# Optimization experiments

Measured on AMD Instinct MI355X. Metric: run time of the kernel, lower is better.

Reference implementation:

```python
import jax, jax.numpy as jnp
import numpy as np

D_IN = 1024
N_HEADS = 16
DEPTH = D_IN // N_HEADS
SCALE = float(np.sqrt(DEPTH))


def setup_inputs() -> dict:
    key = jax.random.key(0)
    ks = jax.random.split(key, 11)
    B, S = 4, 1024
    s = 0.02
    return {
        "q": jax.random.normal(ks[0], (B, S, D_IN), jnp.float32),
        "k": jax.random.normal(ks[1], (B, S, D_IN), jnp.float32),
        "v": jax.random.normal(ks[2], (B, S, D_IN), jnp.float32),
        "mask": jnp.zeros((1, 1, S, S), jnp.float32),
        "wq_w": jax.random.normal(ks[3], (D_IN, D_IN), jnp.float32) * s,
        "wq_b": jax.random.normal(ks[4], (D_IN,), jnp.float32) * s,
        "wk_w": jax.random.normal(ks[5], (D_IN, D_IN), jnp.float32) * s,
        "wk_b": jax.random.normal(ks[6], (D_IN,), jnp.float32) * s,
        "wv_w": jax.random.normal(ks[7], (D_IN, D_IN), jnp.float32) * s,
        "wv_b": jax.random.normal(ks[8], (D_IN,), jnp.float32) * s,
        "pl_w": jax.random.normal(ks[9], (D_IN, D_IN), jnp.float32) * s,
        "pl_b": jax.random.normal(ks[10], (D_IN,), jnp.float32) * s,
    }


def _split_heads(x):
    # [B, S, D] -> [B, H, S, depth]
    B, S, _ = x.shape
    return x.reshape(B, S, N_HEADS, DEPTH).transpose(0, 2, 1, 3)


def reference(q, k, v, mask, wq_w, wq_b, wk_w, wk_b, wv_w, wv_b, pl_w, pl_b):
    # torch Linear: y = x @ W.T + b
    qh = _split_heads(q @ wq_w.T + wq_b)
    kh = _split_heads(k @ wk_w.T + wk_b)
    vh = _split_heads(v @ wv_w.T + wv_b)
    # [B, H, Sq, Sk]
    logits = jnp.einsum("bhqd,bhkd->bhqk", qh, kh) / SCALE
    logits = logits + mask * (-1e9)
    weights = jax.nn.softmax(logits, axis=-1)
    attn = jnp.einsum("bhqk,bhkd->bhqd", weights, vh)
    B = q.shape[0]
    attn = attn.transpose(0, 2, 1, 3).reshape(B, -1, D_IN)
    return attn @ pl_w.T + pl_b
```

## Files before the change

kernel.cpp:

```cpp
#include <hip/hip_runtime.h>
#include <stdint.h>

#define B_ 4
#define S_ 1024
#define DMODEL 1024
#define H_ 16
#define DP_ 64

typedef __attribute__((ext_vector_type(8))) short short8;
typedef __attribute__((ext_vector_type(4))) float floatx4;
typedef __attribute__((ext_vector_type(16))) float floatx16;
typedef __attribute__((ext_vector_type(8))) unsigned short ushort8;
typedef __attribute__((ext_vector_type(4))) unsigned short ushort4v;
typedef __attribute__((ext_vector_type(4))) unsigned int uintx4;

#define LOG2E 1.44269504088896f

__device__ __forceinline__ unsigned short f2bf(float x) {
    union { float f; unsigned int u; } c; c.f = x;
    unsigned int r = c.u + 0x7FFFu + ((c.u >> 16) & 1u);
    return (unsigned short)(r >> 16);
}
__device__ __forceinline__ float bf2f(unsigned short b) {
    union { float f; unsigned int u; } c; c.u = ((unsigned int)b) << 16;
    return c.f;
}
__device__ __forceinline__ unsigned pack2(float lo, float hi) {
    union { float f; unsigned int u; } a, b; a.f = lo; b.f = hi;
    return ((b.u + 0x8000u) & 0xFFFF0000u) | ((a.u + 0x8000u) >> 16);
}

#if __has_builtin(__builtin_amdgcn_exp2f)
#define EXP2(x) __builtin_amdgcn_exp2f(x)
#else
#define EXP2(x) exp2f(x)
#endif

#define GLDS16(gp, lp) __builtin_amdgcn_global_load_lds( \
    (const __attribute__((address_space(1))) void*)(gp),  \
    (__attribute__((address_space(3))) void*)(lp), 16, 0, 0)

__global__ __launch_bounds__(256) void convert_all(
    const float* __restrict__ q, const float* __restrict__ k, const float* __restrict__ v,
    const float* __restrict__ wq, const float* __restrict__ wk, const float* __restrict__ wv,
    const float* __restrict__ wp, const float* __restrict__ mask,
    unsigned short* __restrict__ ws)
{
    const unsigned g = blockIdx.x * 256u + threadIdx.x;
    const float* s; unsigned short* d; unsigned off; float sc = 1.0f;
    if (g < 524288u)        { s = q;  d = ws;            off = g; }
    else if (g < 1048576u)  { s = k;  d = ws + 4194304;  off = g - 524288u; }
    else if (g < 1572864u)  { s = v;  d = ws + 8388608;  off = g - 1048576u; }
    else if (g < 1703936u)  { s = wq; d = ws + 12582912; off = g - 1572864u; }
    else if (g < 1835008u)  { s = wk; d = ws + 13631488; off = g - 1703936u; }
    else if (g < 1966080u)  { s = wv; d = ws + 14680064; off = g - 1835008u; }
    else if (g < 2097152u)  { s = wp; d = ws + 15728640; off = g - 1966080u; }
    else { s = mask; d = ws + 16777216; off = g - 2097152u; sc = -1e9f * LOG2E; }
    const floatx4 a = ((const floatx4*)s)[(size_t)off * 2];
    const floatx4 b = ((const floatx4*)s)[(size_t)off * 2 + 1];
    ushort8 r;
    r[0] = f2bf(a[0] * sc); r[1] = f2bf(a[1] * sc); r[2] = f2bf(a[2] * sc); r[3] = f2bf(a[3] * sc);
    r[4] = f2bf(b[0] * sc); r[5] = f2bf(b[1] * sc); r[6] = f2bf(b[2] * sc); r[7] = f2bf(b[3] * sc);
    ((ushort8*)d)[off] = r;
}

template<bool SWAP>
__device__ __forceinline__ void gemm_body(
    const unsigned short* __restrict__ X, const unsigned short* __restrict__ W,
    const int row0, const int col0,
    unsigned short* Xs, unsigned short* Ws, floatx4* acc)
{
    const int tid = threadIdx.x, w = tid >> 6, lane = tid & 63;
    const int l15 = lane & 15, l4 = lane >> 4;
    const int wr = w >> 1, wc = w & 1;
    const int srow = lane >> 3;
    const int sgrp = (lane & 7) ^ srow;
    auto* XsL = (__attribute__((address_space(3))) unsigned short*)Xs;
    auto* WsL = (__attribute__((address_space(3))) unsigned short*)Ws;

    for (int it = 0; it < 16; it++) {
        const int kk = it * 64;
        __syncthreads();
        for (int j = 0; j < 4; j++) {
            const int rb = w * 32 + j * 8;
            GLDS16(X + (size_t)(row0 + rb + srow) * DMODEL + kk + sgrp * 8, XsL + rb * 64);
            GLDS16(W + (size_t)(col0 + rb + srow) * DMODEL + kk + sgrp * 8, WsL + rb * 64);
        }
        __syncthreads();
        for (int ks = 0; ks < 2; ks++) {
            const int slot = ((ks * 4 + l4) ^ (l15 & 7)) * 8;
            short8 xf[4], wf[4];
            for (int t = 0; t < 4; t++) {
                xf[t] = *(const short8*)(Xs + (wr * 64 + t * 16 + l15) * 64 + slot);
                wf[t] = *(const short8*)(Ws + (wc * 64 + t * 16 + l15) * 64 + slot);
            }
            for (int a = 0; a < 4; a++)
                for (int b2 = 0; b2 < 4; b2++)
                    acc[a * 4 + b2] = SWAP
                        ? __builtin_amdgcn_mfma_f32_16x16x32_bf16(wf[a], xf[b2], acc[a * 4 + b2], 0, 0, 0)
                        : __builtin_amdgcn_mfma_f32_16x16x32_bf16(xf[a], wf[b2], acc[a * 4 + b2], 0, 0, 0);
        }
    }
}

__global__ __launch_bounds__(256, 3) void qkv_gemm(
    const unsigned short* __restrict__ Xall, const unsigned short* __restrict__ Wall,
    const float* __restrict__ bq, const float* __restrict__ bk, const float* __restrict__ bv,
    unsigned short* __restrict__ Qh, unsigned short* __restrict__ Kh,
    unsigned short* __restrict__ Vt)
{
    __shared__ unsigned short Xs[8192];
    __shared__ unsigned short Ws[8192];
    const int sel = blockIdx.y >> 5;
    const int row0 = (blockIdx.y & 31) * 128, col0 = blockIdx.x * 128;
    const unsigned short* X = Xall + (size_t)sel * 4194304;
    const unsigned short* W = Wall + (size_t)sel * 1048576;
    const float* bias = (sel == 0) ? bq : (sel == 1) ? bk : bv;

    const int tid = threadIdx.x, w = tid >> 6, lane = tid & 63;
    const int l15 = lane & 15, l4 = lane >> 4;
    const int wr = w >> 1, wc = w & 1;

    floatx4 acc[16];
    for (int i = 0; i < 16; i++) acc[i] = (floatx4){0.f, 0.f, 0.f, 0.f};

    if (sel < 2) {
        gemm_body<true>(X, W, row0, col0, Xs, Ws, acc);
        unsigned short* Out = sel ? Kh : Qh;
        const float scale = sel ? 1.0f : 0.125f * LOG2E;
        for (int nt = 0; nt < 4; nt++) {
            const int n0 = col0 + wc * 64 + nt * 16 + l4 * 4;
            const floatx4 bv4 = *(const floatx4*)(bias + n0);
            const int h = n0 >> 6, d0 = n0 & 63;
            for (int mt = 0; mt < 4; mt++) {
                const int m = row0 + wr * 64 + mt * 16 + l15;
                const int b = m >> 10, s = m & 1023;
                const floatx4 a = acc[nt * 4 + mt];
                ushort4v pk;
                for (int i = 0; i < 4; i++) pk[i] = f2bf((a[i] + bv4[i]) * scale);
                *(ushort4v*)(Out + (((size_t)(b * H_ + h) * S_ + s) * DP_ + d0)) = pk;
            }
        }
    } else {
        gemm_body<false>(X, W, row0, col0, Xs, Ws, acc);
        for (int mt = 0; mt < 4; mt++) {
            const int m0 = row0 + wr * 64 + mt * 16 + l4 * 4;
            const int b = m0 >> 10, s0 = m0 & 1023;
            for (int nt = 0; nt < 4; nt++) {
                const int n = col0 + wc * 64 + nt * 16 + l15;
                const int h = n >> 6, d = n & 63;
                const float bvv = bias[n];
                const floatx4 a = acc[mt * 4 + nt];
                ushort4v pk;
                for (int i = 0; i < 4; i++) pk[i] = f2bf(a[i] + bvv);
                *(ushort4v*)(Vt + (((size_t)(b * H_ + h) * DP_ + d) * S_ + s0)) = pk;
            }
        }
    }
}

__global__ __launch_bounds__(256, 4) void out_gemm(
    const unsigned short* __restrict__ X, const unsigned short* __restrict__ W,
    const float* __restrict__ bias, float* __restrict__ Out)
{
    __shared__ unsigned short Xs[128 * 64];
    __shared__ unsigned short Ws[64 * 64];
    const int row0 = blockIdx.y * 128, col0 = blockIdx.x * 64;
    const int tid = threadIdx.x, w = tid >> 6, lane = tid & 63;
    const int l15 = lane & 15, l4 = lane >> 4;
    const int srow = lane >> 3, sgrp = (lane & 7) ^ srow;
    auto* XsL = (__attribute__((address_space(3))) unsigned short*)Xs;
    auto* WsL = (__attribute__((address_space(3))) unsigned short*)Ws;

    floatx4 acc[8];
    for (int i = 0; i < 8; i++) acc[i] = (floatx4){0.f, 0.f, 0.f, 0.f};

    for (int it = 0; it < 16; it++) {
        const int kk = it * 64;
        __syncthreads();
        for (int j = 0; j < 4; j++) {
            const int rb = w * 32 + j * 8;
            GLDS16(X + (size_t)(row0 + rb + srow) * DMODEL + kk + sgrp * 8, XsL + rb * 64);
        }
        for (int j = 0; j < 2; j++) {
            const int rb = w * 16 + j * 8;
            GLDS16(W + (size_t)(col0 + rb + srow) * DMODEL + kk + sgrp * 8, WsL + rb * 64);
        }
        __syncthreads();
        for (int ks = 0; ks < 2; ks++) {
            const int slot = ((ks * 4 + l4) ^ (l15 & 7)) * 8;
            short8 xf[2], wf[4];
            for (int t = 0; t < 2; t++)
                xf[t] = *(const short8*)(Xs + (w * 32 + t * 16 + l15) * 64 + slot);
            for (int t = 0; t < 4; t++)
                wf[t] = *(const short8*)(Ws + (t * 16 + l15) * 64 + slot);
            for (int nt = 0; nt < 4; nt++)
                for (int mt = 0; mt < 2; mt++)
                    acc[nt * 2 + mt] = __builtin_amdgcn_mfma_f32_16x16x32_bf16(
                        wf[nt], xf[mt], acc[nt * 2 + mt], 0, 0, 0);
        }
    }

    for (int nt = 0; nt < 4; nt++) {
        const int n0 = col0 + nt * 16 + l4 * 4;
        const floatx4 bv4 = *(const floatx4*)(bias + n0);
        for (int mt = 0; mt < 2; mt++) {
            const int m = row0 + w * 32 + mt * 16 + l15;
            floatx4 ov;
            for (int i = 0; i < 4; i++) ov[i] = acc[nt * 2 + mt][i] + bv4[i];
            *(floatx4*)(Out + (size_t)m * DMODEL + n0) = ov;
        }
    }
}

__global__ __launch_bounds__(256, 4) void attn_fwd(
    const unsigned short* __restrict__ Qh, const unsigned short* __restrict__ Kh,
    const unsigned short* __restrict__ Vt, const unsigned short* __restrict__ maskb,
    unsigned short* __restrict__ attnO)
{
    __shared__ unsigned short Ks[2 * 4096];
    __shared__ unsigned short Vs[2 * 4096];
    auto* KsL = (__attribute__((address_space(3))) unsigned short*)Ks;
    auto* VsL = (__attribute__((address_space(3))) unsigned short*)Vs;

    const int bh = blockIdx.x, qt = blockIdx.y;
    const int b = bh >> 4, h = bh & 15;
    const int tid = threadIdx.x, w = tid >> 6, lane = tid & 63;
    const int l31 = lane & 31, hh = lane >> 5;
    const int qh = w >> 1, kh = w & 1;
    const int srow = lane >> 3, sgrp = (lane & 7) ^ srow;
    const int qg = qt * 64 + qh * 32 + l31;
    const int sw7 = l31 & 7;

    short8 bq[4];
    for (int c = 0; c < 4; c++)
        bq[c] = *(const short8*)(Qh + ((size_t)bh * S_ + qg) * DP_ + c * 16 + hh * 8);

    for (int j = 0; j < 2; j++) {
        const int rb = w * 16 + j * 8;
        GLDS16(Kh + ((size_t)bh * S_ + rb + srow) * DP_ + sgrp * 8, KsL + rb * 64);
        GLDS16(Vt + ((size_t)bh * DP_ + rb + srow) * S_ + sgrp * 8, VsL + rb * 64);
    }
    ushort4v mk[4], mkn[4];
    for (int t = 0; t < 4; t++)
        mk[t] = *(const ushort4v*)(maskb + (size_t)qg * S_ + kh * 32 + t * 8 + hh * 4);

    float l_i = 0.f;
    floatx16 o[2];
    for (int du = 0; du < 2; du++)
        for (int i = 0; i < 16; i++) o[du][i] = 0.f;

    for (int kt = 0; kt < 16; kt++) {
        const int cur = kt & 1, nxt = cur ^ 1;
        __syncthreads();
        if (kt < 15) {
            for (int j = 0; j < 2; j++) {
                const int rb = w * 16 + j * 8;
                GLDS16(Kh + ((size_t)bh * S_ + (kt + 1) * 64 + rb + srow) * DP_ + sgrp * 8,
                       KsL + nxt * 4096 + rb * 64);
                GLDS16(Vt + ((size_t)bh * DP_ + rb + srow) * S_ + (kt + 1) * 64 + sgrp * 8,
                       VsL + nxt * 4096 + rb * 64);
            }
            for (int t = 0; t < 4; t++)
                mkn[t] = *(const ushort4v*)(maskb + (size_t)qg * S_ + (kt + 1) * 64 + kh * 32 + t * 8 + hh * 4);
        }

        const unsigned short* Kc = Ks + cur * 4096;
        const unsigned short* Vc = Vs + cur * 4096;
        floatx16 sa;
        for (int i = 0; i < 16; i++) sa[i] = 0.f;
        for (int c = 0; c < 4; c++) {
            short8 ak = *(const short8*)(Kc + (kh * 32 + l31) * 64 + ((c * 2 + hh) ^ sw7) * 8);
            sa = __builtin_amdgcn_mfma_f32_32x32x16_bf16(ak, bq[c], sa, 0, 0, 0);
        }

        unsigned pd[8];
        for (int t = 0; t < 4; t++) {
            float p0 = EXP2(sa[t * 4 + 0] + bf2f(mk[t][0]));
            float p1 = EXP2(sa[t * 4 + 1] + bf2f(mk[t][1]));
            float p2 = EXP2(sa[t * 4 + 2] + bf2f(mk[t][2]));
            float p3 = EXP2(sa[t * 4 + 3] + bf2f(mk[t][3]));
            l_i += (p0 + p1) + (p2 + p3);
            pd[t * 2 + 0] = pack2(p0, p1);
            pd[t * 2 + 1] = pack2(p2, p3);
        }

        unsigned snd0 = hh ? pd[0] : pd[2];
        unsigned snd1 = hh ? pd[1] : pd[3];
        unsigned snd2 = hh ? pd[4] : pd[6];
        unsigned snd3 = hh ? pd[5] : pd[7];
        unsigned r0 = (unsigned)__shfl_xor((int)snd0, 32, 64);
        unsigned r1 = (unsigned)__shfl_xor((int)snd1, 32, 64);
        unsigned r2 = (unsigned)__shfl_xor((int)snd2, 32, 64);
        unsigned r3 = (unsigned)__shfl_xor((int)snd3, 32, 64);
        uintx4 u0 = { hh ? r0 : pd[0], hh ? r1 : pd[1], hh ? pd[2] : r0, hh ? pd[3] : r1 };
        uintx4 u1 = { hh ? r2 : pd[4], hh ? r3 : pd[5], hh ? pd[6] : r2, hh ? pd[7] : r3 };
        short8 bp[2];
        bp[0] = __builtin_bit_cast(short8, u0);
        bp[1] = __builtin_bit_cast(short8, u1);

        for (int c2 = 0; c2 < 2; c2++)
            for (int du = 0; du < 2; du++) {
                short8 av = *(const short8*)(Vc + (du * 32 + l31) * 64 + ((kh * 4 + c2 * 2 + hh) ^ sw7) * 8);
                o[du] = __builtin_amdgcn_mfma_f32_32x32x16_bf16(av, bp[c2], o[du], 0, 0, 0);
            }

        if (kt < 15)
            for (int t = 0; t < 4; t++) mk[t] = mkn[t];
    }

    __syncthreads();
    l_i += __shfl_xor(l_i, 32, 64);
    float* Lbuf = (float*)(Vs + 4096);
    if (lane < 32) Lbuf[w * 32 + l31] = l_i;

    float* Obuf = (float*)Ks;
    if (kh == 1) {
        for (int du = 0; du < 2; du++)
            for (int rr = 0; rr < 4; rr++) {
                floatx4 v4 = { o[du][rr * 4 + 0], o[du][rr * 4 + 1],
                               o[du][rr * 4 + 2], o[du][rr * 4 + 3] };
                *(floatx4*)(Obuf + qh * 2048 + l31 * 64 +
                            ((du * 8 + rr * 2 + hh) ^ (l31 & 15)) * 4) = v4;
            }
    }
    __syncthreads();

    unsigned short* T = Vs;
    if (kh == 0) {
        const float inv = 1.0f / (Lbuf[(qh * 2) * 32 + l31] + Lbuf[(qh * 2 + 1) * 32 + l31]);
        for (int du = 0; du < 2; du++)
            for (int rr = 0; rr < 4; rr++) {
                floatx4 part = *(const floatx4*)(Obuf + qh * 2048 + l31 * 64 +
                                ((du * 8 + rr * 2 + hh) ^ (l31 & 15)) * 4);
                ushort4v pk;
                for (int i = 0; i < 4; i++)
                    pk[i] = f2bf((o[du][rr * 4 + i] + part[i]) * inv);
                *(ushort4v*)(T + (qh * 32 + l31) * 64 +
                             ((du * 4 + rr) ^ sw7) * 8 + hh * 4) = pk;
            }
    }
    __syncthreads();
    const int r = tid >> 2;
    for (int t = 0; t < 2; t++) {
        const int g = (tid & 3) + t * 4;
        ushort8 ov = *(const ushort8*)(T + r * 64 + ((g ^ (r & 7)) * 8));
        *(ushort8*)(attnO + ((size_t)(b * S_ + qt * 64 + r)) * DMODEL + h * DP_ + g * 8) = ov;
    }
}

extern "C" void kernel_launch(void* const* d_in, const int* in_sizes, int n_in,
                              void* d_out, int out_size, void* d_ws, size_t ws_size,
                              hipStream_t stream)
{
    (void)in_sizes; (void)n_in; (void)out_size; (void)ws_size;
    const float* q    = (const float*)d_in[0];
    const float* k    = (const float*)d_in[1];
    const float* v    = (const float*)d_in[2];
    const float* mask = (const float*)d_in[3];
    const float* wq_w = (const float*)d_in[4];
    const float* wq_b = (const float*)d_in[5];
    const float* wk_w = (const float*)d_in[6];
    const float* wk_b = (const float*)d_in[7];
    const float* wv_w = (const float*)d_in[8];
    const float* wv_b = (const float*)d_in[9];
    const float* pl_w = (const float*)d_in[10];
    const float* pl_b = (const float*)d_in[11];

    unsigned short* ws = (unsigned short*)d_ws;
    unsigned short* Xall  = ws;
    unsigned short* Wall  = ws + 12582912;
    unsigned short* Wp    = ws + 15728640;
    unsigned short* maskb = ws + 16777216;
    unsigned short* Qh    = ws + 17825792;
    unsigned short* Kh    = ws + 22020096;
    unsigned short* Vt    = ws + 4194304;
    unsigned short* attnB = ws;

    dim3 bb(256, 1, 1);
    convert_all<<<dim3(8704, 1, 1), bb, 0, stream>>>(q, k, v, wq_w, wk_w, wv_w, pl_w, mask, ws);
    qkv_gemm<<<dim3(8, 96, 1), bb, 0, stream>>>(Xall, Wall, wq_b, wk_b, wv_b, Qh, Kh, Vt);
    attn_fwd<<<dim3(64, 16, 1), bb, 0, stream>>>(Qh, Kh, Vt, maskb, attnB);
    out_gemm<<<dim3(16, 32, 1), bb, 0, stream>>>(attnB, Wp, pl_b, (float*)d_out);
}
```

Before: 224.7 us.

## Shrink attention blocks, load V directly to registers, stage GEMM output via LDS

The attention kernel now uses 128-thread blocks covering 32 queries, which doubles the grid. V is read straight from global memory into registers, and the LDS double buffer for V is removed. The out GEMM epilogue now stages results through swizzled shared memory so that global stores are row-contiguous and coalesced. The aim is to cut LDS traffic and raise occupancy. The trade-offs are that V no longer has an async prefetch, so its loads can stall at each iteration, and each block now loads K and V for only 32 queries, which doubles the K/V traffic from global memory or L2.

```diff
diff --git a/kernel.cpp b/kernel.cpp
--- a/kernel.cpp
+++ b/kernel.cpp
@@ -201,50 +201,61 @@
         }
     }
 
-    for (int nt = 0; nt < 4; nt++) {
-        const int n0 = col0 + nt * 16 + l4 * 4;
-        const floatx4 bv4 = *(const floatx4*)(bias + n0);
-        for (int mt = 0; mt < 2; mt++) {
-            const int m = row0 + w * 32 + mt * 16 + l15;
-            floatx4 ov;
-            for (int i = 0; i < 4; i++) ov[i] = acc[nt * 2 + mt][i] + bv4[i];
-            *(floatx4*)(Out + (size_t)m * DMODEL + n0) = ov;
-        }
-    }
-}
-
-__global__ __launch_bounds__(256, 4) void attn_fwd(
+    float* Cb = (float*)Xs;
+    for (int c = 0; c < 2; c++) {
+        __syncthreads();
+        if ((w >> 1) == c) {
+            for (int nt = 0; nt < 4; nt++) {
+                const int n0 = col0 + nt * 16 + l4 * 4;
+                const floatx4 bv4 = *(const floatx4*)(bias + n0);
+                for (int mt = 0; mt < 2; mt++) {
+                    const int ml = (w & 1) * 32 + mt * 16 + l15;
+                    floatx4 ov;
+                    for (int i = 0; i < 4; i++) ov[i] = acc[nt * 2 + mt][i] + bv4[i];
+                    *(floatx4*)(Cb + ml * 64 + ((nt * 4 + l4) ^ l15) * 4) = ov;
+                }
+            }
+        }
+        __syncthreads();
+        for (int rnd = 0; rnd < 4; rnd++) {
+            const int r = (tid >> 4) + rnd * 16;
+            const int gs = tid & 15;
+            floatx4 v = *(const floatx4*)(Cb + r * 64 + ((gs ^ (r & 15)) * 4));
+            *(floatx4*)(Out + (size_t)(row0 + c * 64 + r) * DMODEL + col0 + gs * 4) = v;
+        }
+    }
+}
+
+__global__ __launch_bounds__(128, 4) void attn_fwd(
     const unsigned short* __restrict__ Qh, const unsigned short* __restrict__ Kh,
     const unsigned short* __restrict__ Vt, const unsigned short* __restrict__ maskb,
     unsigned short* __restrict__ attnO)
 {
     __shared__ unsigned short Ks[2 * 4096];
-    __shared__ unsigned short Vs[2 * 4096];
     auto* KsL = (__attribute__((address_space(3))) unsigned short*)Ks;
-    auto* VsL = (__attribute__((address_space(3))) unsigned short*)Vs;
 
     const int bh = blockIdx.x, qt = blockIdx.y;
     const int b = bh >> 4, h = bh & 15;
-    const int tid = threadIdx.x, w = tid >> 6, lane = tid & 63;
+    const int tid = threadIdx.x;
+    const int kh = tid >> 6, lane = tid & 63;
     const int l31 = lane & 31, hh = lane >> 5;
-    const int qh = w >> 1, kh = w & 1;
     const int srow = lane >> 3, sgrp = (lane & 7) ^ srow;
-    const int qg = qt * 64 + qh * 32 + l31;
+    const int qg = qt * 32 + l31;
     const int sw7 = l31 & 7;
 
     short8 bq[4];
     for (int c = 0; c < 4; c++)
         bq[c] = *(const short8*)(Qh + ((size_t)bh * S_ + qg) * DP_ + c * 16 + hh * 8);
 
-    for (int j = 0; j < 2; j++) {
-        const int rb = w * 16 + j * 8;
+    for (int j = 0; j < 4; j++) {
+        const int rb = j * 16 + kh * 8;
         GLDS16(Kh + ((size_t)bh * S_ + rb + srow) * DP_ + sgrp * 8, KsL + rb * 64);
-        GLDS16(Vt + ((size_t)bh * DP_ + rb + srow) * S_ + sgrp * 8, VsL + rb * 64);
     }
     ushort4v mk[4], mkn[4];
     for (int t = 0; t < 4; t++)
         mk[t] = *(const ushort4v*)(maskb + (size_t)qg * S_ + kh * 32 + t * 8 + hh * 4);
 
+    const unsigned short* Vbase = Vt + (size_t)bh * DP_ * S_;
     float l_i = 0.f;
     floatx16 o[2];
     for (int du = 0; du < 2; du++)
@@ -253,20 +264,22 @@
     for (int kt = 0; kt < 16; kt++) {
         const int cur = kt & 1, nxt = cur ^ 1;
         __syncthreads();
+        short8 av[4];
+        for (int du = 0; du < 2; du++)
+            for (int c2 = 0; c2 < 2; c2++)
+                av[du * 2 + c2] = *(const short8*)(Vbase + (size_t)(du * 32 + l31) * S_
+                                   + kt * 64 + kh * 32 + c2 * 16 + hh * 8);
         if (kt < 15) {
-            for (int j = 0; j < 2; j++) {
-                const int rb = w * 16 + j * 8;
+            for (int j = 0; j < 4; j++) {
+                const int rb = j * 16 + kh * 8;
                 GLDS16(Kh + ((size_t)bh * S_ + (kt + 1) * 64 + rb + srow) * DP_ + sgrp * 8,
                        KsL + nxt * 4096 + rb * 64);
-                GLDS16(Vt + ((size_t)bh * DP_ + rb + srow) * S_ + (kt + 1) * 64 + sgrp * 8,
-                       VsL + nxt * 4096 + rb * 64);
             }
             for (int t = 0; t < 4; t++)
                 mkn[t] = *(const ushort4v*)(maskb + (size_t)qg * S_ + (kt + 1) * 64 + kh * 32 + t * 8 + hh * 4);
         }
 
         const unsigned short* Kc = Ks + cur * 4096;
-        const unsigned short* Vc = Vs + cur * 4096;
         floatx16 sa;
         for (int i = 0; i < 16; i++) sa[i] = 0.f;
         for (int c = 0; c < 4; c++) {
@@ -300,10 +313,8 @@
         bp[1] = __builtin_bit_cast(short8, u1);
 
         for (int c2 = 0; c2 < 2; c2++)
-            for (int du = 0; du < 2; du++) {
-                short8 av = *(const short8*)(Vc + (du * 32 + l31) * 64 + ((kh * 4 + c2 * 2 + hh) ^ sw7) * 8);
-                o[du] = __builtin_amdgcn_mfma_f32_32x32x16_bf16(av, bp[c2], o[du], 0, 0, 0);
-            }
+            for (int du = 0; du < 2; du++)
+                o[du] = __builtin_amdgcn_mfma_f32_32x32x16_bf16(av[du * 2 + c2], bp[c2], o[du], 0, 0, 0);
 
         if (kt < 15)
             for (int t = 0; t < 4; t++) mk[t] = mkn[t];
@@ -311,41 +322,38 @@
 
     __syncthreads();
     l_i += __shfl_xor(l_i, 32, 64);
-    float* Lbuf = (float*)(Vs + 4096);
-    if (lane < 32) Lbuf[w * 32 + l31] = l_i;
-
     float* Obuf = (float*)Ks;
+    unsigned short* T = Ks + 4096;
+    float* Lbuf = (float*)(Ks + 6144);
+
     if (kh == 1) {
+        if (lane < 32) Lbuf[l31] = l_i;
         for (int du = 0; du < 2; du++)
             for (int rr = 0; rr < 4; rr++) {
                 floatx4 v4 = { o[du][rr * 4 + 0], o[du][rr * 4 + 1],
                                o[du][rr * 4 + 2], o[du][rr * 4 + 3] };
-                *(floatx4*)(Obuf + qh * 2048 + l31 * 64 +
-                            ((du * 8 + rr * 2 + hh) ^ (l31 & 15)) * 4) = v4;
+                *(floatx4*)(Obuf + l31 * 64 + ((du * 8 + rr * 2 + hh) ^ (l31 & 15)) * 4) = v4;
             }
     }
     __syncthreads();
-
-    unsigned short* T = Vs;
     if (kh == 0) {
-        const float inv = 1.0f / (Lbuf[(qh * 2) * 32 + l31] + Lbuf[(qh * 2 + 1) * 32 + l31]);
+        const float inv = 1.0f / (l_i + Lbuf[l31]);
         for (int du = 0; du < 2; du++)
             for (int rr = 0; rr < 4; rr++) {
-                floatx4 part = *(const floatx4*)(Obuf + qh * 2048 + l31 * 64 +
+                floatx4 part = *(const floatx4*)(Obuf + l31 * 64 +
                                 ((du * 8 + rr * 2 + hh) ^ (l31 & 15)) * 4);
                 ushort4v pk;
                 for (int i = 0; i < 4; i++)
                     pk[i] = f2bf((o[du][rr * 4 + i] + part[i]) * inv);
-                *(ushort4v*)(T + (qh * 32 + l31) * 64 +
-                             ((du * 4 + rr) ^ sw7) * 8 + hh * 4) = pk;
+                *(ushort4v*)(T + l31 * 64 + ((du * 4 + rr) ^ sw7) * 8 + hh * 4) = pk;
             }
     }
     __syncthreads();
-    const int r = tid >> 2;
-    for (int t = 0; t < 2; t++) {
-        const int g = (tid & 3) + t * 4;
+    for (int rnd = 0; rnd < 2; rnd++) {
+        const int r = (tid >> 3) + rnd * 16;
+        const int g = tid & 7;
         ushort8 ov = *(const ushort8*)(T + r * 64 + ((g ^ (r & 7)) * 8));
-        *(ushort8*)(attnO + ((size_t)(b * S_ + qt * 64 + r)) * DMODEL + h * DP_ + g * 8) = ov;
+        *(ushort8*)(attnO + ((size_t)(b * S_ + qt * 32 + r)) * DMODEL + h * DP_ + g * 8) = ov;
     }
 }
 
@@ -380,6 +388,6 @@
     dim3 bb(256, 1, 1);
     convert_all<<<dim3(8704, 1, 1), bb, 0, stream>>>(q, k, v, wq_w, wk_w, wv_w, pl_w, mask, ws);
     qkv_gemm<<<dim3(8, 96, 1), bb, 0, stream>>>(Xall, Wall, wq_b, wk_b, wv_b, Qh, Kh, Vt);
-    attn_fwd<<<dim3(64, 16, 1), bb, 0, stream>>>(Qh, Kh, Vt, maskb, attnB);
+    attn_fwd<<<dim3(64, 32, 1), dim3(128, 1, 1), 0, stream>>>(Qh, Kh, Vt, maskb, attnB);
     out_gemm<<<dim3(16, 32, 1), bb, 0, stream>>>(attnB, Wp, pl_b, (float*)d_out);
 }
```

Measured after the change: 244.4 us. 1.09x slower.
